# Kernel optimization log

Measured on AMD Instinct MI355X. Metric: run time of the kernel, lower is better.

Reference implementation:

```python
import jax, jax.numpy as jnp
import numpy as np

N, E, D, K = 100000, 1000000, 64, 2  # nodes, edges, channels, kernel_size (dim=1, degree=1)


def setup_inputs() -> dict:
    key = jax.random.key(0)
    ks = jax.random.split(key, 10)
    x = jax.random.normal(ks[0], (N, D), dtype=jnp.float32)
    edge_index = jax.random.randint(ks[1], (2, E), 0, N, dtype=jnp.int64)
    edge_attr = jax.random.uniform(ks[2], (E, 1), dtype=jnp.float32)
    s = 1.0 / np.sqrt(D)
    W1 = jax.random.uniform(ks[3], (K, D, D), jnp.float32, -s, s)   # spline weights layer1 [K, in, out]
    lw1 = jax.random.uniform(ks[4], (D, D), jnp.float32, -s, s)     # root linear (x @ lw)
    b1 = jnp.zeros((D,), jnp.float32)
    W2 = jax.random.uniform(ks[5], (K, D, D), jnp.float32, -s, s)
    lw2 = jax.random.uniform(ks[6], (D, D), jnp.float32, -s, s)
    b2 = jnp.zeros((D,), jnp.float32)
    return {"x": x, "edge_index": edge_index, "edge_attr": edge_attr,
            "W1": W1, "lw1": lw1, "b1": b1, "W2": W2, "lw2": lw2, "b2": b2}


def spline_conv(x, src, dst, u, W, lw, b):
    # dim=1, degree=1, open B-spline: v = u*(K-1); linear interp between kernels floor(v), floor(v)+1
    k = W.shape[0]
    v = u[:, 0] * (k - 1)
    i0 = jnp.clip(jnp.floor(v), 0, k - 1).astype(jnp.int32)
    frac = v - i0.astype(v.dtype)            # in [0,1); 0 at u==1 after clipping
    i1 = jnp.minimum(i0 + 1, k - 1)
    Z = jnp.einsum('ni,kio->nko', x, W)      # [N, K, out] precompute per-kernel transforms
    msg = (1.0 - frac)[:, None] * Z[src, i0] + frac[:, None] * Z[src, i1]  # [E, out]
    agg = jax.ops.segment_sum(msg, dst, num_segments=x.shape[0])
    cnt = jax.ops.segment_sum(jnp.ones_like(dst, dtype=x.dtype), dst, num_segments=x.shape[0])
    out = agg / jnp.maximum(cnt, 1.0)[:, None]   # mean aggregation
    return out + x @ lw + b                      # root weight + bias


def reference(x, edge_index, edge_attr, W1, lw1, b1, W2, lw2, b2):
    src, dst = edge_index[0], edge_index[1]
    h = spline_conv(x, src, dst, edge_attr, W1, lw1, b1)
    h = jax.nn.relu(h)                 # dropout is identity in eval mode
    h = spline_conv(h, src, dst, edge_attr, W2, lw2, b2)
    h = jax.nn.relu(h)
    return h
```

## Files before the change

kernel.cpp:

```cpp
#include <hip/hip_runtime.h>

#define TPB 256

typedef __attribute__((ext_vector_type(8))) short bf16x8;
typedef __attribute__((ext_vector_type(4))) float f32x4;

#define CPAD 16

__device__ __forceinline__ float bf2f(unsigned short u) {
    unsigned int x = ((unsigned int)u) << 16;
    return __builtin_bit_cast(float, x);
}
__device__ __forceinline__ unsigned short f2bf(float f) {
    unsigned int u = __builtin_bit_cast(unsigned int, f);
    unsigned int r = u + 0x7FFFu + ((u >> 16) & 1u);
    return (unsigned short)(r >> 16);
}

__global__ void prep_kernel(const float* __restrict__ x, uint2* __restrict__ xb, int n4,
                            const float* __restrict__ W1, const float* __restrict__ lw1,
                            const float* __restrict__ W2, const float* __restrict__ lw2,
                            bf16x8* __restrict__ WA,
                            const int* __restrict__ dst, const int* __restrict__ src,
                            const float* __restrict__ u, int* __restrict__ countsPad,
                            uint2* __restrict__ cp, int E) {
    int t = blockIdx.x * TPB + threadIdx.x;
    if (t < 3072) {
        int which = t / 1536;
        int rem = t - which * 1536;
        int fragid = rem >> 6;
        int lane = rem & 63;
        int kk = fragid >> 2, ct = fragid & 3;
        const float* W  = which ? W2  : W1;
        const float* lw = which ? lw2 : lw1;
        int col = ct * 16 + (lane & 15);
        int kbase = kk * 32 + (lane >> 4) * 8;
        short vals[8];
#pragma unroll
        for (int j = 0; j < 8; ++j) {
            int k = kbase + j;
            float v = (k < 128) ? W[(k & 1) * 4096 + (k >> 1) * 64 + col]
                                : lw[(k - 128) * 64 + col];
            vals[j] = (short)f2bf(v);
        }
        WA[t] = *reinterpret_cast<bf16x8*>(vals);
    }
    if (t < n4) {
        float4 v = reinterpret_cast<const float4*>(x)[t];
        uint2 r;
        r.x = (unsigned int)f2bf(v.x) | ((unsigned int)f2bf(v.y) << 16);
        r.y = (unsigned int)f2bf(v.z) | ((unsigned int)f2bf(v.w) << 16);
        xb[t] = r;
    }
    if (t < E) {
        int d = dst[t];
        int r = atomicAdd(&countsPad[(size_t)d * CPAD], 1);
        unsigned int uq = (unsigned int)__float2int_rn(u[t] * 32767.f);
        cp[t] = make_uint2((unsigned int)d | ((unsigned int)r << 17),
                           (unsigned int)src[t] | (uq << 17));
    }
}

__global__ void scan1_kernel(const int* __restrict__ countsPad, int* __restrict__ offsets,
                             int* __restrict__ bsum, int n) {
    __shared__ int s[TPB];
    int t = threadIdx.x;
    int base = blockIdx.x * 1024 + t * 4;
    int v[4];
#pragma unroll
    for (int q = 0; q < 4; ++q) v[q] = (base + q < n) ? countsPad[(size_t)(base + q) * CPAD] : 0;
    int tsum = v[0] + v[1] + v[2] + v[3];
    s[t] = tsum;
    __syncthreads();
    for (int off = 1; off < TPB; off <<= 1) {
        int x = (t >= off) ? s[t - off] : 0;
        __syncthreads();
        s[t] += x;
        __syncthreads();
    }
    int acc = s[t] - tsum;
#pragma unroll
    for (int q = 0; q < 4; ++q) {
        if (base + q < n) offsets[base + q] = acc;
        acc += v[q];
    }
    if (t == TPB - 1) bsum[blockIdx.x] = s[TPB - 1];
}

__global__ void scan2_kernel(int* __restrict__ bsum, int nblk) {
    __shared__ int s[TPB];
    int t = threadIdx.x;
    int v = (t < nblk) ? bsum[t] : 0;
    s[t] = v;
    __syncthreads();
    for (int off = 1; off < TPB; off <<= 1) {
        int x = (t >= off) ? s[t - off] : 0;
        __syncthreads();
        s[t] += x;
        __syncthreads();
    }
    if (t < nblk) bsum[t] = s[t] - v;
}

__global__ void scan3_kernel(int* __restrict__ offsets, const int* __restrict__ bsum,
                             int n, int E) {
    int base = blockIdx.x * 1024 + threadIdx.x * 4;
    int add = bsum[blockIdx.x];
#pragma unroll
    for (int q = 0; q < 4; ++q) {
        int idx = base + q;
        if (idx < n) offsets[idx] += add;
    }
    if (blockIdx.x == 0 && threadIdx.x == 0) offsets[n] = E;
}

__global__ void fill_kernel(const uint2* __restrict__ cp,
                            const int* __restrict__ offsets,
                            unsigned int* __restrict__ csr, int E, int nphases) {
    int stride = gridDim.x * TPB;
    for (int p = 0; p < nphases; ++p) {
        for (int e = blockIdx.x * TPB + threadIdx.x; e < E; e += stride) {
            uint2 r = cp[e];
            int d = r.x & 0x1FFFF;
            if ((d >> 16) == p) {
                int pos = offsets[d] + (int)(r.x >> 17);
                csr[pos] = r.y;
            }
        }
    }
}

__global__ void agg_kernel(const unsigned int* __restrict__ featu,
                           const int* __restrict__ offsets,
                           const unsigned int* __restrict__ csr,
                           unsigned int* __restrict__ A, int N) {
    int gw = (blockIdx.x * TPB + threadIdx.x) >> 6;
    int lane = threadIdx.x & 63;
    if (gw >= N) return;
    int beg = offsets[gw], end = offsets[gw + 1];
    int cnt = end - beg;
    int half = lane >> 5, sub = lane & 31;
    const float us = 1.f / 32767.f;

    unsigned int cw = (lane < cnt) ? csr[beg + lane] : 0u;

    float a0x = 0.f, a1x = 0.f, a0y = 0.f, a1y = 0.f;
    int npre = cnt < 64 ? cnt : 64;
    int npair = npre >> 1;
    int j = 0;

#define PAIR_MATH(C, F)                                                        \
    {                                                                          \
        float uu = (float)((C) >> 17) * us;                                    \
        float w0 = 1.f - uu;                                                   \
        float fx = bf2f((unsigned short)(F));                                  \
        float fy = bf2f((unsigned short)((F) >> 16));                          \
        a0x = fmaf(fx, w0, a0x); a1x = fmaf(fx, uu, a1x);                      \
        a0y = fmaf(fy, w0, a0y); a1y = fmaf(fy, uu, a1y);                      \
    }

    for (; j + 4 <= npair; j += 4) {
        unsigned int c0 = __shfl(cw, 2 * j     + half);
        unsigned int c1 = __shfl(cw, 2 * j + 2 + half);
        unsigned int c2 = __shfl(cw, 2 * j + 4 + half);
        unsigned int c3 = __shfl(cw, 2 * j + 6 + half);
        unsigned int f0 = featu[(size_t)(c0 & 0x1FFFF) * 32 + sub];
        unsigned int f1 = featu[(size_t)(c1 & 0x1FFFF) * 32 + sub];
        unsigned int f2 = featu[(size_t)(c2 & 0x1FFFF) * 32 + sub];
        unsigned int f3 = featu[(size_t)(c3 & 0x1FFFF) * 32 + sub];
        PAIR_MATH(c0, f0); PAIR_MATH(c1, f1); PAIR_MATH(c2, f2); PAIR_MATH(c3, f3);
    }
    for (; j < npair; ++j) {
        unsigned int c0 = __shfl(cw, 2 * j + half);
        unsigned int f0 = featu[(size_t)(c0 & 0x1FFFF) * 32 + sub];
        PAIR_MATH(c0, f0);
    }
    if (npre & 1) {
        unsigned int c0 = __shfl(cw, npre - 1);
        unsigned int f0 = featu[(size_t)(c0 & 0x1FFFF) * 32 + sub];
        float uu = (float)(c0 >> 17) * us;
        float w0 = (half == 0) ? 1.f - uu : 0.f;
        float w1 = (half == 0) ? uu : 0.f;
        float fx = bf2f((unsigned short)f0);
        float fy = bf2f((unsigned short)(f0 >> 16));
        a0x = fmaf(fx, w0, a0x); a1x = fmaf(fx, w1, a1x);
        a0y = fmaf(fy, w0, a0y); a1y = fmaf(fy, w1, a1y);
    }
    for (int jj = 64 + half; jj < cnt; jj += 2) {
        unsigned int c0 = csr[beg + jj];
        unsigned int f0 = featu[(size_t)(c0 & 0x1FFFF) * 32 + sub];
        PAIR_MATH(c0, f0);
    }
#undef PAIR_MATH

    a0x += __shfl_xor(a0x, 32); a1x += __shfl_xor(a1x, 32);
    a0y += __shfl_xor(a0y, 32); a1y += __shfl_xor(a1y, 32);
    float inv = 1.f / (float)(cnt > 0 ? cnt : 1);
    if (half == 0) {
        uint2 pk;
        pk.x = (unsigned int)f2bf(a0x * inv) | ((unsigned int)f2bf(a1x * inv) << 16);
        pk.y = (unsigned int)f2bf(a0y * inv) | ((unsigned int)f2bf(a1y * inv) << 16);
        *reinterpret_cast<uint2*>(A + (size_t)gw * 64 + sub * 2) = pk;
    }
}

__global__ void gemm_mfma_kernel(const unsigned int* __restrict__ A,
                                 const unsigned short* __restrict__ feat,
                                 const bf16x8* __restrict__ WA,
                                 const float* __restrict__ bias,
                                 unsigned short* __restrict__ out_bf,
                                 float* __restrict__ out_f,
                                 int N, int write_f32) {
    int w = threadIdx.x >> 6, lane = threadIdx.x & 63;
    int node = blockIdx.x * 64 + w * 16 + (lane & 15);
    int nc = min(node, N - 1);
    int kq = lane >> 4;
    const char* arow = (const char*)A + (size_t)nc * 256 + kq * 16;
    const char* frow = (const char*)feat + (size_t)nc * 128 + kq * 16;
    bf16x8 bq[6];
    bq[0] = *(const bf16x8*)(arow);
    bq[1] = *(const bf16x8*)(arow + 64);
    bq[2] = *(const bf16x8*)(arow + 128);
    bq[3] = *(const bf16x8*)(arow + 192);
    bq[4] = *(const bf16x8*)(frow);
    bq[5] = *(const bf16x8*)(frow + 64);

    f32x4 acc0 = {0.f, 0.f, 0.f, 0.f}, acc1 = acc0, acc2 = acc0, acc3 = acc0;
#pragma unroll
    for (int kk = 0; kk < 6; ++kk) {
        bf16x8 b = bq[kk];
        acc0 = __builtin_amdgcn_mfma_f32_16x16x32_bf16(WA[(kk * 4 + 0) * 64 + lane], b, acc0, 0, 0, 0);
        acc1 = __builtin_amdgcn_mfma_f32_16x16x32_bf16(WA[(kk * 4 + 1) * 64 + lane], b, acc1, 0, 0, 0);
        acc2 = __builtin_amdgcn_mfma_f32_16x16x32_bf16(WA[(kk * 4 + 2) * 64 + lane], b, acc2, 0, 0, 0);
        acc3 = __builtin_amdgcn_mfma_f32_16x16x32_bf16(WA[(kk * 4 + 3) * 64 + lane], b, acc3, 0, 0, 0);
    }
    if (node >= N) return;

    f32x4 accs[4] = {acc0, acc1, acc2, acc3};
    int cb_hi = 4 * kq;
#pragma unroll
    for (int ct = 0; ct < 4; ++ct) {
        int cb = ct * 16 + cb_hi;
        float r0 = fmaxf(accs[ct][0] + bias[cb + 0], 0.f);
        float r1 = fmaxf(accs[ct][1] + bias[cb + 1], 0.f);
        float r2 = fmaxf(accs[ct][2] + bias[cb + 2], 0.f);
        float r3 = fmaxf(accs[ct][3] + bias[cb + 3], 0.f);
        if (write_f32) {
            *reinterpret_cast<float4*>(out_f + (size_t)node * 64 + cb) =
                make_float4(r0, r1, r2, r3);
        } else {
            uint2 pk;
            pk.x = (unsigned int)f2bf(r0) | ((unsigned int)f2bf(r1) << 16);
            pk.y = (unsigned int)f2bf(r2) | ((unsigned int)f2bf(r3) << 16);
            *reinterpret_cast<uint2*>(out_bf + (size_t)node * 64 + cb) = pk;
        }
    }
}

extern "C" void kernel_launch(void* const* d_in, const int* in_sizes, int n_in,
                              void* d_out, int out_size, void* d_ws, size_t ws_size,
                              hipStream_t stream) {
    const float* x   = (const float*)d_in[0];
    const int*   ei  = (const int*)d_in[1];
    const float* ea  = (const float*)d_in[2];
    const float* W1  = (const float*)d_in[3];
    const float* lw1 = (const float*)d_in[4];
    const float* b1  = (const float*)d_in[5];
    const float* W2  = (const float*)d_in[6];
    const float* lw2 = (const float*)d_in[7];
    const float* b2  = (const float*)d_in[8];

    const int N = in_sizes[0] / 64;
    const int E = in_sizes[1] / 2;

    char* p = (char*)d_ws;
    auto carve = [&](size_t bytes) -> void* {
        void* r = (void*)p;
        p += (bytes + 255) & ~(size_t)255;
        return r;
    };
    unsigned short* xb   = (unsigned short*)carve((size_t)N * 64 * 2);
    unsigned short* h    = (unsigned short*)carve((size_t)N * 64 * 2);
    unsigned int*   A    = (unsigned int*)carve((size_t)N * 64 * 4);
    bf16x8* WA      = (bf16x8*)carve(3072 * 16);
    int*   countsPad = (int*)carve((size_t)N * CPAD * 4);
    int*   offsets  = (int*)carve((size_t)(N + 1) * 4);
    int*   bsum     = (int*)carve(256 * 4);
    uint2* cp       = (uint2*)carve((size_t)E * 8);
    unsigned int* csr = (unsigned int*)carve((size_t)E * 4);

    const int* src = ei;
    const int* dst = ei + E;

    hipMemsetAsync(countsPad, 0, (size_t)N * CPAD * 4, stream);

    int n4 = N * 64 / 4;
    int prepTotal = n4 > E ? n4 : E;
    prep_kernel<<<(prepTotal + TPB - 1) / TPB, TPB, 0, stream>>>(
        x, (uint2*)xb, n4, W1, lw1, W2, lw2, WA, dst, src, ea, countsPad, cp, E);

    int nscan = (N + 1023) / 1024;
    scan1_kernel<<<nscan, TPB, 0, stream>>>(countsPad, offsets, bsum, N);
    scan2_kernel<<<1, TPB, 0, stream>>>(bsum, nscan);
    scan3_kernel<<<nscan, TPB, 0, stream>>>(offsets, bsum, N, E);

    int eBlocks = (E + TPB - 1) / TPB;
    int nphases = (N + 65535) >> 16;
    fill_kernel<<<eBlocks, TPB, 0, stream>>>(cp, offsets, csr, E, nphases);

    int aBlocks = (N + 3) / 4;
    int gBlocks = (N + 63) / 64;

    agg_kernel<<<aBlocks, TPB, 0, stream>>>((const unsigned int*)xb, offsets, csr, A, N);
    gemm_mfma_kernel<<<gBlocks, TPB, 0, stream>>>(A, xb, WA, b1, h, nullptr, N, 0);
    agg_kernel<<<aBlocks, TPB, 0, stream>>>((const unsigned int*)h, offsets, csr, A, N);
    gemm_mfma_kernel<<<gBlocks, TPB, 0, stream>>>(A, h, WA + 1536, b2, nullptr, (float*)d_out, N, 1);
}
```

Baseline: 179.4 us.

## Process two nodes per wave in aggregation and drop padded degree counters

The aggregation kernel now assigns two destination nodes to each 64-lane wave. It loads both nodes' CSR entries with a single coalesced read, issues up to 16 feature gathers per node up front, and then reduces each node separately, with a fallback loop for high-degree nodes. Separately, the per-node degree counters are no longer padded to 16 ints, which shrinks the memset and the scan reads but puts more atomic contention on shared cache lines. The intent is more memory-level parallelism and fewer idle lanes per wave, since the average degree is about 10. The cost is higher register use and masked, wasted gathers for low-degree nodes.

```diff
diff --git a/kernel.cpp b/kernel.cpp
--- a/kernel.cpp
+++ b/kernel.cpp
@@ -4,8 +4,6 @@
 
 typedef __attribute__((ext_vector_type(8))) short bf16x8;
 typedef __attribute__((ext_vector_type(4))) float f32x4;
-
-#define CPAD 16
 
 __device__ __forceinline__ float bf2f(unsigned short u) {
     unsigned int x = ((unsigned int)u) << 16;
@@ -22,7 +20,7 @@
                             const float* __restrict__ W2, const float* __restrict__ lw2,
                             bf16x8* __restrict__ WA,
                             const int* __restrict__ dst, const int* __restrict__ src,
-                            const float* __restrict__ u, int* __restrict__ countsPad,
+                            const float* __restrict__ u, int* __restrict__ counts,
                             uint2* __restrict__ cp, int E) {
     int t = blockIdx.x * TPB + threadIdx.x;
     if (t < 3072) {
@@ -54,21 +52,21 @@
     }
     if (t < E) {
         int d = dst[t];
-        int r = atomicAdd(&countsPad[(size_t)d * CPAD], 1);
+        int r = atomicAdd(&counts[d], 1);
         unsigned int uq = (unsigned int)__float2int_rn(u[t] * 32767.f);
         cp[t] = make_uint2((unsigned int)d | ((unsigned int)r << 17),
                            (unsigned int)src[t] | (uq << 17));
     }
 }
 
-__global__ void scan1_kernel(const int* __restrict__ countsPad, int* __restrict__ offsets,
+__global__ void scan1_kernel(const int* __restrict__ counts, int* __restrict__ offsets,
                              int* __restrict__ bsum, int n) {
     __shared__ int s[TPB];
     int t = threadIdx.x;
     int base = blockIdx.x * 1024 + t * 4;
     int v[4];
 #pragma unroll
-    for (int q = 0; q < 4; ++q) v[q] = (base + q < n) ? countsPad[(size_t)(base + q) * CPAD] : 0;
+    for (int q = 0; q < 4; ++q) v[q] = (base + q < n) ? counts[base + q] : 0;
     int tsum = v[0] + v[1] + v[2] + v[3];
     s[t] = tsum;
     __syncthreads();
@@ -136,71 +134,78 @@
                            unsigned int* __restrict__ A, int N) {
     int gw = (blockIdx.x * TPB + threadIdx.x) >> 6;
     int lane = threadIdx.x & 63;
-    if (gw >= N) return;
-    int beg = offsets[gw], end = offsets[gw + 1];
-    int cnt = end - beg;
+    int n0 = gw * 2;
+    if (n0 >= N) return;
     int half = lane >> 5, sub = lane & 31;
     const float us = 1.f / 32767.f;
 
+    int ov = offsets[min(n0 + (lane & 3), N)];
+    int o0 = __shfl(ov, 0), o1 = __shfl(ov, 1), o2 = __shfl(ov, 2);
+    int beg = o0;
+    int cnt = o2 - o0;
     unsigned int cw = (lane < cnt) ? csr[beg + lane] : 0u;
 
-    float a0x = 0.f, a1x = 0.f, a0y = 0.f, a1y = 0.f;
-    int npre = cnt < 64 ? cnt : 64;
-    int npair = npre >> 1;
-    int j = 0;
-
-#define PAIR_MATH(C, F)                                                        \
-    {                                                                          \
-        float uu = (float)((C) >> 17) * us;                                    \
-        float w0 = 1.f - uu;                                                   \
-        float fx = bf2f((unsigned short)(F));                                  \
-        float fy = bf2f((unsigned short)((F) >> 16));                          \
-        a0x = fmaf(fx, w0, a0x); a1x = fmaf(fx, uu, a1x);                      \
-        a0y = fmaf(fy, w0, a0y); a1y = fmaf(fy, uu, a1y);                      \
-    }
-
-    for (; j + 4 <= npair; j += 4) {
-        unsigned int c0 = __shfl(cw, 2 * j     + half);
-        unsigned int c1 = __shfl(cw, 2 * j + 2 + half);
-        unsigned int c2 = __shfl(cw, 2 * j + 4 + half);
-        unsigned int c3 = __shfl(cw, 2 * j + 6 + half);
-        unsigned int f0 = featu[(size_t)(c0 & 0x1FFFF) * 32 + sub];
-        unsigned int f1 = featu[(size_t)(c1 & 0x1FFFF) * 32 + sub];
-        unsigned int f2 = featu[(size_t)(c2 & 0x1FFFF) * 32 + sub];
-        unsigned int f3 = featu[(size_t)(c3 & 0x1FFFF) * 32 + sub];
-        PAIR_MATH(c0, f0); PAIR_MATH(c1, f1); PAIR_MATH(c2, f2); PAIR_MATH(c3, f3);
-    }
-    for (; j < npair; ++j) {
-        unsigned int c0 = __shfl(cw, 2 * j + half);
-        unsigned int f0 = featu[(size_t)(c0 & 0x1FFFF) * 32 + sub];
-        PAIR_MATH(c0, f0);
-    }
-    if (npre & 1) {
-        unsigned int c0 = __shfl(cw, npre - 1);
-        unsigned int f0 = featu[(size_t)(c0 & 0x1FFFF) * 32 + sub];
-        float uu = (float)(c0 >> 17) * us;
-        float w0 = (half == 0) ? 1.f - uu : 0.f;
-        float w1 = (half == 0) ? uu : 0.f;
-        float fx = bf2f((unsigned short)f0);
-        float fy = bf2f((unsigned short)(f0 >> 16));
-        a0x = fmaf(fx, w0, a0x); a1x = fmaf(fx, w1, a1x);
-        a0y = fmaf(fy, w0, a0y); a1y = fmaf(fy, w1, a1y);
-    }
-    for (int jj = 64 + half; jj < cnt; jj += 2) {
-        unsigned int c0 = csr[beg + jj];
-        unsigned int f0 = featu[(size_t)(c0 & 0x1FFFF) * 32 + sub];
-        PAIR_MATH(c0, f0);
-    }
-#undef PAIR_MATH
-
-    a0x += __shfl_xor(a0x, 32); a1x += __shfl_xor(a1x, 32);
-    a0y += __shfl_xor(a0y, 32); a1y += __shfl_xor(a1y, 32);
-    float inv = 1.f / (float)(cnt > 0 ? cnt : 1);
-    if (half == 0) {
-        uint2 pk;
-        pk.x = (unsigned int)f2bf(a0x * inv) | ((unsigned int)f2bf(a1x * inv) << 16);
-        pk.y = (unsigned int)f2bf(a0y * inv) | ((unsigned int)f2bf(a1y * inv) << 16);
-        *reinterpret_cast<uint2*>(A + (size_t)gw * 64 + sub * 2) = pk;
+    int S0 = 0, E0 = o1 - o0;
+    int S1 = E0, E1 = cnt;
+
+    unsigned int fb[16], cs[16];
+#pragma unroll
+    for (int i = 0; i < 2; ++i) {
+        int si = i ? S1 : S0;
+        int ei = i ? E1 : E0;
+        int bend = min(min(ei, si + 16), 64);
+#pragma unroll
+        for (int q = 0; q < 8; ++q) {
+            int eidx = si + 2 * q + half;
+            bool v = eidx < bend;
+            unsigned int c = __shfl(cw, v ? eidx : 0);
+            cs[i * 8 + q] = c;
+            fb[i * 8 + q] = featu[(size_t)(c & 0x1FFFF) * 32 + sub];
+        }
+    }
+
+#pragma unroll
+    for (int i = 0; i < 2; ++i) {
+        int si = i ? S1 : S0;
+        int ei = i ? E1 : E0;
+        int bend = min(min(ei, si + 16), 64);
+        float a0x = 0.f, a1x = 0.f, a0y = 0.f, a1y = 0.f;
+#pragma unroll
+        for (int q = 0; q < 8; ++q) {
+            int eidx = si + 2 * q + half;
+            float m = (eidx < bend) ? 1.f : 0.f;
+            unsigned int c = cs[i * 8 + q];
+            unsigned int f = fb[i * 8 + q];
+            float uu = (float)(c >> 17) * us;
+            float w1 = uu * m;
+            float w0 = m - w1;
+            float fx = bf2f((unsigned short)f);
+            float fy = bf2f((unsigned short)(f >> 16));
+            a0x = fmaf(fx, w0, a0x); a1x = fmaf(fx, w1, a1x);
+            a0y = fmaf(fy, w0, a0y); a1y = fmaf(fy, w1, a1y);
+        }
+        int tstart = max(si, bend);
+        for (int t = tstart + half; t < ei; t += 2) {
+            unsigned int c = csr[beg + t];
+            unsigned int f = featu[(size_t)(c & 0x1FFFF) * 32 + sub];
+            float uu = (float)(c >> 17) * us;
+            float w0 = 1.f - uu;
+            float fx = bf2f((unsigned short)f);
+            float fy = bf2f((unsigned short)(f >> 16));
+            a0x = fmaf(fx, w0, a0x); a1x = fmaf(fx, uu, a1x);
+            a0y = fmaf(fy, w0, a0y); a1y = fmaf(fy, uu, a1y);
+        }
+        a0x += __shfl_xor(a0x, 32); a1x += __shfl_xor(a1x, 32);
+        a0y += __shfl_xor(a0y, 32); a1y += __shfl_xor(a1y, 32);
+        int node = n0 + i;
+        int cN = ei - si;
+        float inv = 1.f / (float)(cN > 0 ? cN : 1);
+        if (half == 0 && node < N) {
+            uint2 pk;
+            pk.x = (unsigned int)f2bf(a0x * inv) | ((unsigned int)f2bf(a1x * inv) << 16);
+            pk.y = (unsigned int)f2bf(a0y * inv) | ((unsigned int)f2bf(a1y * inv) << 16);
+            *reinterpret_cast<uint2*>(A + (size_t)node * 64 + sub * 2) = pk;
+        }
     }
 }
 
@@ -283,7 +288,7 @@
     unsigned short* h    = (unsigned short*)carve((size_t)N * 64 * 2);
     unsigned int*   A    = (unsigned int*)carve((size_t)N * 64 * 4);
     bf16x8* WA      = (bf16x8*)carve(3072 * 16);
-    int*   countsPad = (int*)carve((size_t)N * CPAD * 4);
+    int*   counts   = (int*)carve((size_t)N * 4);
     int*   offsets  = (int*)carve((size_t)(N + 1) * 4);
     int*   bsum     = (int*)carve(256 * 4);
     uint2* cp       = (uint2*)carve((size_t)E * 8);
@@ -292,15 +297,15 @@
     const int* src = ei;
     const int* dst = ei + E;
 
-    hipMemsetAsync(countsPad, 0, (size_t)N * CPAD * 4, stream);
+    hipMemsetAsync(counts, 0, (size_t)N * 4, stream);
 
     int n4 = N * 64 / 4;
     int prepTotal = n4 > E ? n4 : E;
     prep_kernel<<<(prepTotal + TPB - 1) / TPB, TPB, 0, stream>>>(
-        x, (uint2*)xb, n4, W1, lw1, W2, lw2, WA, dst, src, ea, countsPad, cp, E);
+        x, (uint2*)xb, n4, W1, lw1, W2, lw2, WA, dst, src, ea, counts, cp, E);
 
     int nscan = (N + 1023) / 1024;
-    scan1_kernel<<<nscan, TPB, 0, stream>>>(countsPad, offsets, bsum, N);
+    scan1_kernel<<<nscan, TPB, 0, stream>>>(counts, offsets, bsum, N);
     scan2_kernel<<<1, TPB, 0, stream>>>(bsum, nscan);
     scan3_kernel<<<nscan, TPB, 0, stream>>>(offsets, bsum, N, E);
 
@@ -308,7 +313,8 @@
     int nphases = (N + 65535) >> 16;
     fill_kernel<<<eBlocks, TPB, 0, stream>>>(cp, offsets, csr, E, nphases);
 
-    int aBlocks = (N + 3) / 4;
+    int nwaves = (N + 1) / 2;
+    int aBlocks = (nwaves + 3) / 4;
     int gBlocks = (N + 63) / 64;
 
     agg_kernel<<<aBlocks, TPB, 0, stream>>>((const unsigned int*)xb, offsets, csr, A, N);
```

New measurement: 166.8 us. 7.0% less time.
